# Performance work log

Hardware: AMD Instinct MI355X
Metric: run time of the kernel (lower is better)

## Reference

```python
import jax, jax.numpy as jnp
import numpy as np

EPS = 1e-8
H = 4      # n_heads
W = 64     # mem_word_length


def _split_controls(controls):
    # per-head partition: [W, W, W, 1, 1, 3, 1]
    B = controls.shape[0]
    sizes = [W, W, W, 1, 1, 3, 1]
    parts, pos = [], 0
    for s in sizes:
        n = H * s
        parts.append(controls[:, pos:pos + n].reshape(B, H, s))
        pos += n
    return parts  # keys, erase_vec, write_vec, betas, gates, shifts, gammas


def _address_memory(memory, keys, betas, gates, shifts, gammas, prev_weights):
    keys = jnp.tanh(keys)                      # [B,H,W]
    betas = jax.nn.softplus(betas)             # [B,H,1]
    gates = jax.nn.sigmoid(gates)              # [B,H,1]
    shifts = jax.nn.softmax(shifts, axis=-1)   # [B,H,3]
    gammas = 1.0 + jax.nn.softplus(gammas)     # [B,H,1]

    # cosine similarity: [B,H,N]
    dots = jnp.einsum('bhw,bnw->bhn', keys, memory)
    norm = jnp.linalg.norm(keys, axis=-1, keepdims=True) \
         * jnp.linalg.norm(memory, axis=-1)[:, None, :]
    scores = dots / (norm + EPS)

    w_content = jax.nn.softmax(scores * betas, axis=-1)            # [B,H,N]
    w_interp = gates * w_content + (1.0 - gates) * prev_weights    # [B,H,N]

    # circular 3-tap shift: out[n] = s0*w[n-1] + s1*w[n] + s2*w[n+1]
    w_shift = (shifts[..., 0:1] * jnp.roll(w_interp, 1, axis=-1)
             + shifts[..., 1:2] * w_interp
             + shifts[..., 2:3] * jnp.roll(w_interp, -1, axis=-1))

    w_sharp = w_shift ** gammas
    return w_sharp / (jnp.sum(w_sharp, axis=-1, keepdims=True) + EPS)


def reference(memory, controls, prev_weights):
    keys, erase_vec, write_vec, betas, gates, shifts, gammas = _split_controls(controls)
    write_dist = _address_memory(memory, keys, betas, gates, shifts, gammas, prev_weights)  # [B,H,N]
    write_data = jnp.tanh(write_vec)       # [B,H,W]
    erase_data = jax.nn.sigmoid(erase_vec) # [B,H,W]

    # erase: prod over heads of (1 - w[b,h,n]*e[b,h,w]) -> [B,N,W]
    erase_matrix = jnp.prod(1.0 - write_dist[:, :, :, None] * erase_data[:, :, None, :], axis=1)
    update_matrix = jnp.einsum('bhn,bhw->bnw', write_dist, write_data)
    return memory * erase_matrix + update_matrix


def setup_inputs() -> dict:
    key = jax.random.key(0)
    k1, k2, k3 = jax.random.split(key, 3)
    B, N = 64, 8192
    memory = jax.random.normal(k1, (B, N, W), dtype=jnp.float32)
    controls = jax.random.normal(k2, (B, H * (3 * W + 6)), dtype=jnp.float32)
    prev_weights = jax.random.uniform(k3, (B, H, N), dtype=jnp.float32)
    return {"memory": memory, "controls": controls, "prev_weights": prev_weights}
```

## Files before the change

### kernel.cpp

```cpp
#include <hip/hip_runtime.h>
#include <math.h>

#define EPS 1e-8f

__device__ __forceinline__ float softplus_f(float x) {
    return (x > 20.0f) ? x : log1pf(expf(x));
}
__device__ __forceinline__ float sigmoid_f(float x) {
    return 1.0f / (1.0f + expf(-x));
}

__global__ void prep_kernel(const float* __restrict__ controls,
                            float* __restrict__ keys,
                            float* __restrict__ params,
                            float* __restrict__ erase,
                            float* __restrict__ writev)
{
    int b = blockIdx.x;
    int t = threadIdx.x;
    int h = t >> 6;
    int w = t & 63;
    const float* c = controls + (size_t)b * 792;

    float kt = tanhf(c[h * 64 + w]);
    int bh = b * 4 + h;
    keys[bh * 64 + w]   = kt;
    erase[bh * 64 + w]  = sigmoid_f(c[256 + h * 64 + w]);
    writev[bh * 64 + w] = tanhf(c[512 + h * 64 + w]);

    float nsq = kt * kt;
    #pragma unroll
    for (int m = 1; m < 64; m <<= 1) nsq += __shfl_xor(nsq, m, 64);

    if (w == 0) {
        float beta  = softplus_f(c[768 + h]);
        float gate  = sigmoid_f(c[772 + h]);
        float r0 = c[776 + h * 3 + 0];
        float r1 = c[776 + h * 3 + 1];
        float r2 = c[776 + h * 3 + 2];
        float mx = fmaxf(r0, fmaxf(r1, r2));
        float e0 = expf(r0 - mx), e1 = expf(r1 - mx), e2 = expf(r2 - mx);
        float inv = 1.0f / (e0 + e1 + e2);
        float gamma = 1.0f + softplus_f(c[788 + h]);
        float* p = params + bh * 8;
        p[0] = beta; p[1] = gate;
        p[2] = e0 * inv; p[3] = e1 * inv; p[4] = e2 * inv;
        p[5] = gamma; p[6] = sqrtf(nsq); p[7] = 0.0f;
    }
}

__global__ __launch_bounds__(256)
void score_kernel(const float* __restrict__ memory,
                  const float* __restrict__ keys,
                  const float* __restrict__ params,
                  float* __restrict__ scores, int N)
{
    int b = blockIdx.y;
    int nbase = blockIdx.x * 64;
    int t = threadIdx.x;
    int rq = t >> 4;
    int lane = t & 15;

    __shared__ float kk[256];
    __shared__ float betas[4], knorm[4];
    __shared__ float sc[4][64];

    kk[t] = keys[(size_t)b * 256 + t];
    if (t < 4) {
        betas[t] = params[((size_t)b * 4 + t) * 8 + 0];
        knorm[t] = params[((size_t)b * 4 + t) * 8 + 6];
    }
    __syncthreads();

    float4 k4[4];
    #pragma unroll
    for (int h = 0; h < 4; h++) k4[h] = ((const float4*)(kk + h * 64))[lane];

    float4 m4[4];
    #pragma unroll
    for (int j = 0; j < 4; j++) {
        int n = nbase + rq + 16 * j;
        m4[j] = ((const float4*)(memory + ((size_t)b * N + n) * 64))[lane];
    }

    #pragma unroll
    for (int j = 0; j < 4; j++) {
        float nsq = m4[j].x * m4[j].x + m4[j].y * m4[j].y
                  + m4[j].z * m4[j].z + m4[j].w * m4[j].w;
        float d[4];
        #pragma unroll
        for (int h = 0; h < 4; h++) {
            d[h] = m4[j].x * k4[h].x + m4[j].y * k4[h].y
                 + m4[j].z * k4[h].z + m4[j].w * k4[h].w;
        }
        #pragma unroll
        for (int m = 1; m < 16; m <<= 1) {
            nsq += __shfl_xor(nsq, m, 64);
            #pragma unroll
            for (int h = 0; h < 4; h++) d[h] += __shfl_xor(d[h], m, 64);
        }
        if (lane == 0) {
            float mn = sqrtf(nsq);
            int row = rq + 16 * j;
            #pragma unroll
            for (int h = 0; h < 4; h++)
                sc[h][row] = betas[h] * d[h] / (mn * knorm[h] + EPS);
        }
    }
    __syncthreads();
    scores[((size_t)b * 4 + (t >> 6)) * N + nbase + (t & 63)] = sc[t >> 6][t & 63];
}

__device__ __forceinline__ float block_reduce_sum(float v, float* red) {
    #pragma unroll
    for (int m = 1; m < 64; m <<= 1) v += __shfl_xor(v, m, 64);
    int wid = threadIdx.x >> 6;
    __syncthreads();
    if ((threadIdx.x & 63) == 0) red[wid] = v;
    __syncthreads();
    float r = red[0];
    #pragma unroll
    for (int i = 1; i < 16; i++) r += red[i];
    return r;
}
__device__ __forceinline__ float block_reduce_max(float v, float* red) {
    #pragma unroll
    for (int m = 1; m < 64; m <<= 1) v = fmaxf(v, __shfl_xor(v, m, 64));
    int wid = threadIdx.x >> 6;
    __syncthreads();
    if ((threadIdx.x & 63) == 0) red[wid] = v;
    __syncthreads();
    float r = red[0];
    #pragma unroll
    for (int i = 1; i < 16; i++) r = fmaxf(r, red[i]);
    return r;
}

__global__ __launch_bounds__(1024)
void weights_kernel(float* __restrict__ scores,
                    const float* __restrict__ prev,
                    const float* __restrict__ params, int N)
{
    int bh = blockIdx.x;
    int t = threadIdx.x;
    const float* p = params + (size_t)bh * 8;
    float gate = p[1], s0 = p[2], s1 = p[3], s2 = p[4], gamma = p[5];

    __shared__ float wi_s[8192];
    __shared__ float red[16];

    float* srow = scores + (size_t)bh * N;
    const float* prow = prev + (size_t)bh * N;
    int half = N >> 1;
    int i0 = 4 * t, i1 = half + 4 * t;

    float4 sa = ((const float4*)srow)[t];
    float4 sb = ((const float4*)srow)[half / 4 + t];
    float4 pa = ((const float4*)prow)[t];
    float4 pb = ((const float4*)prow)[half / 4 + t];

    float mx = fmaxf(fmaxf(fmaxf(sa.x, sa.y), fmaxf(sa.z, sa.w)),
                     fmaxf(fmaxf(sb.x, sb.y), fmaxf(sb.z, sb.w)));
    mx = block_reduce_max(mx, red);

    float ea[4] = { __expf(sa.x - mx), __expf(sa.y - mx), __expf(sa.z - mx), __expf(sa.w - mx) };
    float eb[4] = { __expf(sb.x - mx), __expf(sb.y - mx), __expf(sb.z - mx), __expf(sb.w - mx) };
    float lsum = ea[0] + ea[1] + ea[2] + ea[3] + eb[0] + eb[1] + eb[2] + eb[3];
    float S = block_reduce_sum(lsum, red);
    float invS = 1.0f / S;

    float og = 1.0f - gate;
    float pv_a[4] = { pa.x, pa.y, pa.z, pa.w };
    float pv_b[4] = { pb.x, pb.y, pb.z, pb.w };
    #pragma unroll
    for (int k = 0; k < 4; k++) {
        wi_s[i0 + k] = gate * (ea[k] * invS) + og * pv_a[k];
        wi_s[i1 + k] = gate * (eb[k] * invS) + og * pv_b[k];
    }
    __syncthreads();

    float wsv[8]; float lsum2 = 0.0f;
    #pragma unroll
    for (int c = 0; c < 2; c++) {
        int base = (c == 0) ? i0 : i1;
        #pragma unroll
        for (int k = 0; k < 4; k++) {
            int i = base + k;
            int im1 = (i == 0) ? (N - 1) : (i - 1);
            int ip1 = (i == N - 1) ? 0 : (i + 1);
            float ws = s0 * wi_s[im1] + s1 * wi_s[i] + s2 * wi_s[ip1];
            float wp = __expf(gamma * __logf(ws));
            wsv[c * 4 + k] = wp; lsum2 += wp;
        }
    }
    float T = block_reduce_sum(lsum2, red);
    float invT = 1.0f / (T + EPS);

    float4 oa = make_float4(wsv[0] * invT, wsv[1] * invT, wsv[2] * invT, wsv[3] * invT);
    float4 ob = make_float4(wsv[4] * invT, wsv[5] * invT, wsv[6] * invT, wsv[7] * invT);
    ((float4*)srow)[t] = oa;
    ((float4*)srow)[half / 4 + t] = ob;
}

__global__ __launch_bounds__(256)
void output_kernel(const float* __restrict__ memory,
                   const float* __restrict__ wdist,
                   const float* __restrict__ erase,
                   const float* __restrict__ writev,
                   float* __restrict__ out, int N)
{
    int t = threadIdx.x;
    int blocksPerB = N >> 6;
    int b = blockIdx.x / blocksPerB;
    int nbase = (blockIdx.x % blocksPerB) << 6;

    __shared__ float es[256], wv[256], wd_s[256];
    es[t] = erase[(size_t)b * 256 + t];
    wv[t] = writev[(size_t)b * 256 + t];
    wd_s[t] = wdist[((size_t)b * 4 + (t >> 6)) * N + nbase + (t & 63)];
    __syncthreads();

    int rq = t >> 4, lane = t & 15;

    float4 e4[4], w4[4];
    #pragma unroll
    for (int h = 0; h < 4; h++) {
        e4[h] = ((const float4*)(es + h * 64))[lane];
        w4[h] = ((const float4*)(wv + h * 64))[lane];
    }

    float4 m4[4];
    #pragma unroll
    for (int j = 0; j < 4; j++) {
        int n = nbase + rq + 16 * j;
        m4[j] = ((const float4*)(memory + ((size_t)b * N + n) * 64))[lane];
    }

    #pragma unroll
    for (int j = 0; j < 4; j++) {
        int row = rq + 16 * j;
        int n = nbase + row;
        float4 pe = make_float4(1.f, 1.f, 1.f, 1.f);
        float4 up = make_float4(0.f, 0.f, 0.f, 0.f);
        #pragma unroll
        for (int h = 0; h < 4; h++) {
            float f = wd_s[h * 64 + row];
            pe.x *= 1.0f - f * e4[h].x;  pe.y *= 1.0f - f * e4[h].y;
            pe.z *= 1.0f - f * e4[h].z;  pe.w *= 1.0f - f * e4[h].w;
            up.x += f * w4[h].x;  up.y += f * w4[h].y;
            up.z += f * w4[h].z;  up.w += f * w4[h].w;
        }
        float4 o;
        o.x = m4[j].x * pe.x + up.x;
        o.y = m4[j].y * pe.y + up.y;
        o.z = m4[j].z * pe.z + up.z;
        o.w = m4[j].w * pe.w + up.w;
        ((float4*)(out + ((size_t)b * N + n) * 64))[lane] = o;
    }
}

extern "C" void kernel_launch(void* const* d_in, const int* in_sizes, int n_in,
                              void* d_out, int out_size, void* d_ws, size_t ws_size,
                              hipStream_t stream) {
    const float* memory   = (const float*)d_in[0];
    const float* controls = (const float*)d_in[1];
    const float* prev     = (const float*)d_in[2];
    float* out = (float*)d_out;

    int B = in_sizes[1] / 792;
    int N = in_sizes[0] / (B * 64);

    float* wsf    = (float*)d_ws;
    float* keys   = wsf;
    float* params = keys   + (size_t)B * 256;
    float* erase  = params + (size_t)B * 32;
    float* writev = erase  + (size_t)B * 256;
    float* scores = writev + (size_t)B * 256;

    prep_kernel<<<B, 256, 0, stream>>>(controls, keys, params, erase, writev);
    score_kernel<<<dim3(N / 64, B), 256, 0, stream>>>(memory, keys, params, scores, N);
    weights_kernel<<<B * 4, 1024, 0, stream>>>(scores, prev, params, N);
    output_kernel<<<B * (N / 64), 256, 0, stream>>>(memory, scores, erase, writev, out, N);
}
```

Baseline: 271.7 us.

## Fuse prep into consumers, double rows per block, use nontemporal output stores

Removes the separate prep kernel and recomputes the control transforms (tanh keys, key norms, betas, gate, shift softmax, gamma, erase and write vectors) inside each consuming kernel. This saves a launch and a workspace round trip. Score and output kernels now handle 128 rows per block instead of 64, giving more loads in flight per thread and fewer blocks. Output stores become nontemporal so the 134MB result does not pollute cache. The cost is redundant transcendental work in every block and higher register pressure from 8 float4 memory rows per thread.

New measurement: 269.0 us. No clear change (-1.0%).

```diff
diff --git a/kernel.cpp b/kernel.cpp
--- a/kernel.cpp
+++ b/kernel.cpp
@@ -3,6 +3,8 @@
 
 #define EPS 1e-8f
 
+typedef float nfloat4 __attribute__((ext_vector_type(4)));
+
 __device__ __forceinline__ float softplus_f(float x) {
     return (x > 20.0f) ? x : log1pf(expf(x));
 }
@@ -10,81 +12,52 @@
     return 1.0f / (1.0f + expf(-x));
 }
 
-__global__ void prep_kernel(const float* __restrict__ controls,
-                            float* __restrict__ keys,
-                            float* __restrict__ params,
-                            float* __restrict__ erase,
-                            float* __restrict__ writev)
-{
-    int b = blockIdx.x;
-    int t = threadIdx.x;
-    int h = t >> 6;
-    int w = t & 63;
-    const float* c = controls + (size_t)b * 792;
-
-    float kt = tanhf(c[h * 64 + w]);
-    int bh = b * 4 + h;
-    keys[bh * 64 + w]   = kt;
-    erase[bh * 64 + w]  = sigmoid_f(c[256 + h * 64 + w]);
-    writev[bh * 64 + w] = tanhf(c[512 + h * 64 + w]);
-
-    float nsq = kt * kt;
-    #pragma unroll
-    for (int m = 1; m < 64; m <<= 1) nsq += __shfl_xor(nsq, m, 64);
-
-    if (w == 0) {
-        float beta  = softplus_f(c[768 + h]);
-        float gate  = sigmoid_f(c[772 + h]);
-        float r0 = c[776 + h * 3 + 0];
-        float r1 = c[776 + h * 3 + 1];
-        float r2 = c[776 + h * 3 + 2];
-        float mx = fmaxf(r0, fmaxf(r1, r2));
-        float e0 = expf(r0 - mx), e1 = expf(r1 - mx), e2 = expf(r2 - mx);
-        float inv = 1.0f / (e0 + e1 + e2);
-        float gamma = 1.0f + softplus_f(c[788 + h]);
-        float* p = params + bh * 8;
-        p[0] = beta; p[1] = gate;
-        p[2] = e0 * inv; p[3] = e1 * inv; p[4] = e2 * inv;
-        p[5] = gamma; p[6] = sqrtf(nsq); p[7] = 0.0f;
-    }
-}
 
 __global__ __launch_bounds__(256)
 void score_kernel(const float* __restrict__ memory,
-                  const float* __restrict__ keys,
-                  const float* __restrict__ params,
+                  const float* __restrict__ controls,
                   float* __restrict__ scores, int N)
 {
     int b = blockIdx.y;
-    int nbase = blockIdx.x * 64;
+    int nbase = blockIdx.x * 128;
     int t = threadIdx.x;
     int rq = t >> 4;
     int lane = t & 15;
 
     __shared__ float kk[256];
-    __shared__ float betas[4], knorm[4];
-    __shared__ float sc[4][64];
-
-    kk[t] = keys[(size_t)b * 256 + t];
-    if (t < 4) {
-        betas[t] = params[((size_t)b * 4 + t) * 8 + 0];
-        knorm[t] = params[((size_t)b * 4 + t) * 8 + 6];
+    __shared__ float betas_s[4], knorm_s[4];
+    __shared__ float sc[4][128];
+
+    const float* c = controls + (size_t)b * 792;
+
+    {
+        int h = t >> 6, w = t & 63;
+        float kt = tanhf(c[h * 64 + w]);
+        kk[h * 64 + w] = kt;
+        float nsq = kt * kt;
+        #pragma unroll
+        for (int m = 1; m < 64; m <<= 1) nsq += __shfl_xor(nsq, m, 64);
+        if (w == 0) knorm_s[h] = sqrtf(nsq);
+        if (t < 4)  betas_s[t] = softplus_f(c[768 + t]);
     }
     __syncthreads();
 
     float4 k4[4];
     #pragma unroll
     for (int h = 0; h < 4; h++) k4[h] = ((const float4*)(kk + h * 64))[lane];
-
-    float4 m4[4];
-    #pragma unroll
-    for (int j = 0; j < 4; j++) {
+    float beta_l[4], knorm_l[4];
+    #pragma unroll
+    for (int h = 0; h < 4; h++) { beta_l[h] = betas_s[h]; knorm_l[h] = knorm_s[h]; }
+
+    float4 m4[8];
+    #pragma unroll
+    for (int j = 0; j < 8; j++) {
         int n = nbase + rq + 16 * j;
         m4[j] = ((const float4*)(memory + ((size_t)b * N + n) * 64))[lane];
     }
 
     #pragma unroll
-    for (int j = 0; j < 4; j++) {
+    for (int j = 0; j < 8; j++) {
         float nsq = m4[j].x * m4[j].x + m4[j].y * m4[j].y
                   + m4[j].z * m4[j].z + m4[j].w * m4[j].w;
         float d[4];
@@ -104,11 +77,16 @@
             int row = rq + 16 * j;
             #pragma unroll
             for (int h = 0; h < 4; h++)
-                sc[h][row] = betas[h] * d[h] / (mn * knorm[h] + EPS);
-        }
-    }
-    __syncthreads();
-    scores[((size_t)b * 4 + (t >> 6)) * N + nbase + (t & 63)] = sc[t >> 6][t & 63];
+                sc[h][row] = beta_l[h] * d[h] / (mn * knorm_l[h] + EPS);
+        }
+    }
+    __syncthreads();
+    #pragma unroll
+    for (int k = 0; k < 2; k++) {
+        int idx = t + k * 256;
+        int h = idx >> 7, i = idx & 127;
+        scores[((size_t)b * 4 + h) * N + nbase + i] = sc[h][i];
+    }
 }
 
 __device__ __forceinline__ float block_reduce_sum(float v, float* red) {
@@ -139,12 +117,22 @@
 __global__ __launch_bounds__(1024)
 void weights_kernel(float* __restrict__ scores,
                     const float* __restrict__ prev,
-                    const float* __restrict__ params, int N)
+                    const float* __restrict__ controls, int N)
 {
     int bh = blockIdx.x;
+    int b = bh >> 2, h = bh & 3;
     int t = threadIdx.x;
-    const float* p = params + (size_t)bh * 8;
-    float gate = p[1], s0 = p[2], s1 = p[3], s2 = p[4], gamma = p[5];
+    const float* c = controls + (size_t)b * 792;
+
+    float gate  = sigmoid_f(c[772 + h]);
+    float r0 = c[776 + h * 3 + 0];
+    float r1 = c[776 + h * 3 + 1];
+    float r2 = c[776 + h * 3 + 2];
+    float rmx = fmaxf(r0, fmaxf(r1, r2));
+    float e0 = expf(r0 - rmx), e1 = expf(r1 - rmx), e2 = expf(r2 - rmx);
+    float sinv = 1.0f / (e0 + e1 + e2);
+    float s0 = e0 * sinv, s1 = e1 * sinv, s2 = e2 * sinv;
+    float gamma = 1.0f + softplus_f(c[788 + h]);
 
     __shared__ float wi_s[8192];
     __shared__ float red[16];
@@ -181,8 +169,8 @@
 
     float wsv[8]; float lsum2 = 0.0f;
     #pragma unroll
-    for (int c = 0; c < 2; c++) {
-        int base = (c == 0) ? i0 : i1;
+    for (int cc = 0; cc < 2; cc++) {
+        int base = (cc == 0) ? i0 : i1;
         #pragma unroll
         for (int k = 0; k < 4; k++) {
             int i = base + k;
@@ -190,7 +178,7 @@
             int ip1 = (i == N - 1) ? 0 : (i + 1);
             float ws = s0 * wi_s[im1] + s1 * wi_s[i] + s2 * wi_s[ip1];
             float wp = __expf(gamma * __logf(ws));
-            wsv[c * 4 + k] = wp; lsum2 += wp;
+            wsv[cc * 4 + k] = wp; lsum2 += wp;
         }
     }
     float T = block_reduce_sum(lsum2, red);
@@ -205,19 +193,24 @@
 __global__ __launch_bounds__(256)
 void output_kernel(const float* __restrict__ memory,
                    const float* __restrict__ wdist,
-                   const float* __restrict__ erase,
-                   const float* __restrict__ writev,
+                   const float* __restrict__ controls,
                    float* __restrict__ out, int N)
 {
     int t = threadIdx.x;
-    int blocksPerB = N >> 6;
+    int blocksPerB = N >> 7;
     int b = blockIdx.x / blocksPerB;
-    int nbase = (blockIdx.x % blocksPerB) << 6;
-
-    __shared__ float es[256], wv[256], wd_s[256];
-    es[t] = erase[(size_t)b * 256 + t];
-    wv[t] = writev[(size_t)b * 256 + t];
-    wd_s[t] = wdist[((size_t)b * 4 + (t >> 6)) * N + nbase + (t & 63)];
+    int nbase = (blockIdx.x % blocksPerB) << 7;
+
+    __shared__ float es[256], wv[256], wd_s[512];
+    const float* c = controls + (size_t)b * 792;
+    es[t] = sigmoid_f(c[256 + t]);
+    wv[t] = tanhf(c[512 + t]);
+    #pragma unroll
+    for (int k = 0; k < 2; k++) {
+        int idx = t + k * 256;
+        int h = idx >> 7, i = idx & 127;
+        wd_s[idx] = wdist[((size_t)b * 4 + h) * N + nbase + i];
+    }
     __syncthreads();
 
     int rq = t >> 4, lane = t & 15;
@@ -229,33 +222,34 @@
         w4[h] = ((const float4*)(wv + h * 64))[lane];
     }
 
-    float4 m4[4];
-    #pragma unroll
-    for (int j = 0; j < 4; j++) {
+    float4 m4[8];
+    #pragma unroll
+    for (int j = 0; j < 8; j++) {
         int n = nbase + rq + 16 * j;
         m4[j] = ((const float4*)(memory + ((size_t)b * N + n) * 64))[lane];
     }
 
     #pragma unroll
-    for (int j = 0; j < 4; j++) {
+    for (int j = 0; j < 8; j++) {
         int row = rq + 16 * j;
         int n = nbase + row;
         float4 pe = make_float4(1.f, 1.f, 1.f, 1.f);
         float4 up = make_float4(0.f, 0.f, 0.f, 0.f);
         #pragma unroll
         for (int h = 0; h < 4; h++) {
-            float f = wd_s[h * 64 + row];
+            float f = wd_s[h * 128 + row];
             pe.x *= 1.0f - f * e4[h].x;  pe.y *= 1.0f - f * e4[h].y;
             pe.z *= 1.0f - f * e4[h].z;  pe.w *= 1.0f - f * e4[h].w;
             up.x += f * w4[h].x;  up.y += f * w4[h].y;
             up.z += f * w4[h].z;  up.w += f * w4[h].w;
         }
-        float4 o;
+        nfloat4 o;
         o.x = m4[j].x * pe.x + up.x;
         o.y = m4[j].y * pe.y + up.y;
         o.z = m4[j].z * pe.z + up.z;
         o.w = m4[j].w * pe.w + up.w;
-        ((float4*)(out + ((size_t)b * N + n) * 64))[lane] = o;
+        nfloat4* op = ((nfloat4*)(out + ((size_t)b * N + n) * 64)) + lane;
+        __builtin_nontemporal_store(o, op);
     }
 }
 
@@ -270,15 +264,9 @@
     int B = in_sizes[1] / 792;
     int N = in_sizes[0] / (B * 64);
 
-    float* wsf    = (float*)d_ws;
-    float* keys   = wsf;
-    float* params = keys   + (size_t)B * 256;
-    float* erase  = params + (size_t)B * 32;
-    float* writev = erase  + (size_t)B * 256;
-    float* scores = writev + (size_t)B * 256;
-
-    prep_kernel<<<B, 256, 0, stream>>>(controls, keys, params, erase, writev);
-    score_kernel<<<dim3(N / 64, B), 256, 0, stream>>>(memory, keys, params, scores, N);
-    weights_kernel<<<B * 4, 1024, 0, stream>>>(scores, prev, params, N);
-    output_kernel<<<B * (N / 64), 256, 0, stream>>>(memory, scores, erase, writev, out, N);
-}
+    float* scores = (float*)d_ws;
+
+    score_kernel<<<dim3(N / 128, B), 256, 0, stream>>>(memory, controls, scores, N);
+    weights_kernel<<<B * 4, 1024, 0, stream>>>(scores, prev, controls, N);
+    output_kernel<<<B * (N / 128), 256, 0, stream>>>(memory, scores, controls, out, N);
+}
```
